# Optimization experiments

Measured on AMD Instinct MI355X. Metric: run time of the kernel, lower is better.

Reference implementation:

```python
import jax, jax.numpy as jnp
import numpy as np

CH = 512
HEADS = 4
GROUPS = 32  # _groups(512) -> 32
EPS = 1e-5


def setup_inputs() -> dict:
    key = jax.random.key(0)
    ks = jax.random.split(key, 7)
    b, c, h, w = 16, CH, 32, 32
    sd = 1.0 / np.sqrt(c)
    return {
        "x": jax.random.normal(ks[0], (b, c, h, w), dtype=jnp.float32),
        "gamma": jnp.ones((c,), jnp.float32),
        "beta": jnp.zeros((c,), jnp.float32),
        "w_qkv": jax.random.normal(ks[1], (3 * c, c), dtype=jnp.float32) * sd,
        "b_qkv": jax.random.normal(ks[2], (3 * c,), dtype=jnp.float32) * 0.01,
        "w_proj": jax.random.normal(ks[3], (c, c), dtype=jnp.float32) * sd,
        "b_proj": jax.random.normal(ks[4], (c,), dtype=jnp.float32) * 0.01,
    }


def _group_norm(x, gamma, beta):
    b, c, h, w = x.shape
    xg = x.reshape(b, GROUPS, -1)  # (b, G, c//G * h * w)
    mu = jnp.mean(xg, axis=-1, keepdims=True)
    var = jnp.var(xg, axis=-1, keepdims=True)
    xn = ((xg - mu) * jax.lax.rsqrt(var + EPS)).reshape(b, c, h, w)
    return xn * gamma[None, :, None, None] + beta[None, :, None, None]


def reference(x, gamma, beta, w_qkv, b_qkv, w_proj, b_proj):
    b, c, h, w = x.shape
    hd = c // HEADS
    xn = _group_norm(x, gamma, beta)
    # 1x1 conv == channel matmul
    qkv = jnp.einsum('oc,bchw->bohw', w_qkv, xn) + b_qkv[None, :, None, None]
    qkv = qkv.reshape(b, 3, HEADS, hd, h * w)
    q, k, v = qkv[:, 0], qkv[:, 1], qkv[:, 2]  # (b, H, hd, n)
    scale = hd ** -0.5
    attn = jax.nn.softmax(jnp.einsum('bhcn,bhcm->bhnm', q * scale, k), axis=-1)
    out = jnp.einsum('bhnm,bhcm->bhcn', attn, v).reshape(b, c, h, w)
    out = jnp.einsum('oc,bchw->bohw', w_proj, out) + b_proj[None, :, None, None]
    return x + out
```

## Files before the change

kernel.cpp:

```cpp
#include <hip/hip_runtime.h>

#define CH 512
#define HEADS 4
#define HD 128
#define NPIX 1024
#define BATCH 16
#define GROUPS 32
#define GSZ 16
#define EPS 1e-5f

typedef _Float16 f16;
typedef _Float16 f16x8 __attribute__((ext_vector_type(8)));
typedef _Float16 f16x4 __attribute__((ext_vector_type(4)));
typedef float f32x4 __attribute__((ext_vector_type(4)));

__device__ __forceinline__ void gld16(const f16* g, f16* l) {
    __builtin_amdgcn_global_load_lds((__attribute__((address_space(1))) const void*)g,
                                     (__attribute__((address_space(3))) void*)l, 16, 0, 0);
}

__global__ __launch_bounds__(256, 2) void k_pre(const float* __restrict__ x, const float* __restrict__ gamma,
                                                const float* __restrict__ beta, f16* __restrict__ xnT,
                                                const float* __restrict__ wq, const float* __restrict__ wp,
                                                f16* __restrict__ wqT, f16* __restrict__ wpT) {
    __shared__ float xs[GSZ * NPIX];
    __shared__ float red[8];
    __shared__ float stat2[2];
    int bidx = blockIdx.x;
    if (bidx >= 512) {
        int c = (bidx - 512) * 256 + threadIdx.x;
        {
            int ot = c >> 13, kbl = (c >> 7) & 63, ol = c & 127;
            const float* s = wq + ((size_t)(ot * 128 + ol)) * CH + kbl * 8;
            f32x4 a = *(const f32x4*)s, b2 = *(const f32x4*)(s + 4);
            f16x8 v;
            v[0] = (f16)a.x; v[1] = (f16)a.y; v[2] = (f16)a.z; v[3] = (f16)a.w;
            v[4] = (f16)b2.x; v[5] = (f16)b2.y; v[6] = (f16)b2.z; v[7] = (f16)b2.w;
            *(f16x8*)(wqT + (size_t)c * 8) = v;
        }
        if (c < 32768) {
            int ot = c >> 13, kbl = (c >> 7) & 63, ol = c & 127;
            const float* s = wp + ((size_t)(ot * 128 + ol)) * CH + kbl * 8;
            f32x4 a = *(const f32x4*)s, b2 = *(const f32x4*)(s + 4);
            f16x8 v;
            v[0] = (f16)a.x; v[1] = (f16)a.y; v[2] = (f16)a.z; v[3] = (f16)a.w;
            v[4] = (f16)b2.x; v[5] = (f16)b2.y; v[6] = (f16)b2.z; v[7] = (f16)b2.w;
            *(f16x8*)(wpT + (size_t)c * 8) = v;
        }
        return;
    }
    int g = bidx & 31, b = bidx >> 5;
    const f32x4* x4 = (const f32x4*)(x + ((size_t)(b * GROUPS + g)) * (GSZ * NPIX));
    float s = 0.f, ss = 0.f;
    for (int i = threadIdx.x; i < GSZ * NPIX / 4; i += 256) {
        f32x4 v = x4[i];
        *(f32x4*)&xs[i * 4] = v;
        s  += v.x + v.y + v.z + v.w;
        ss += v.x * v.x + v.y * v.y + v.z * v.z + v.w * v.w;
    }
    for (int off = 32; off; off >>= 1) { s += __shfl_down(s, off); ss += __shfl_down(ss, off); }
    int wv = threadIdx.x >> 6, ln = threadIdx.x & 63;
    if (ln == 0) { red[wv] = s; red[4 + wv] = ss; }
    __syncthreads();
    if (threadIdx.x == 0) {
        float S = red[0] + red[1] + red[2] + red[3];
        float SS = red[4] + red[5] + red[6] + red[7];
        float mu = S / (GSZ * NPIX);
        float var = SS / (GSZ * NPIX) - mu * mu;
        stat2[0] = mu; stat2[1] = rsqrtf(var + EPS);
    }
    __syncthreads();
    float mu = stat2[0], rstd = stat2[1];
    int ch = threadIdx.x >> 7;
    int n  = threadIdx.x & 127;
    float gl[8], bl[8];
#pragma unroll
    for (int i = 0; i < 8; i++) {
        float gv = gamma[g * 16 + ch * 8 + i] * rstd;
        gl[i] = gv;
        bl[i] = beta[g * 16 + ch * 8 + i] - mu * gv;
    }
    f16* tb0 = xnT + ((size_t)(b * 8)) * 65536 + (g * 2 + ch) * 1024 + n * 8;
#pragma unroll
    for (int nt = 0; nt < 8; nt++) {
        f16x8 o;
#pragma unroll
        for (int i = 0; i < 8; i++)
            o[i] = (f16)(xs[(ch * 8 + i) * 1024 + nt * 128 + n] * gl[i] + bl[i]);
        *(f16x8*)(tb0 + (size_t)nt * 65536) = o;
    }
}

__global__ __launch_bounds__(256, 3) void k_qkv(const f16* __restrict__ wT, const float* __restrict__ bias,
                                                const f16* __restrict__ xnT, f16* __restrict__ qF,
                                                f16* __restrict__ kTl, f16* __restrict__ vTl) {
    int nt = blockIdx.x, ot = blockIdx.y, b = blockIdx.z;
    int o0 = ot * 128;
    __shared__ union SM {
        struct { f16 As[8192]; f16 Bs[8192]; } s;
        f16 Cf[16384];
    } sm;
    __shared__ float biasS[128];
    if (threadIdx.x < 128) biasS[threadIdx.x] = bias[o0 + threadIdx.x];
    int tid = threadIdx.x, lane = tid & 63, wv = tid >> 6;
    int wr = wv >> 1, wc = wv & 1;
    int l15 = lane & 15, quad = lane >> 4;
    const f16* wA = wT + (size_t)ot * 65536;
    const f16* xB = xnT + ((size_t)(b * 8 + nt)) * 65536;
    f32x4 acc[4][4] = {};
    for (int kk = 0; kk < CH; kk += 64) {
        __syncthreads();
        const f16* sa = wA + (size_t)(kk >> 3) * 1024;
        const f16* sb = xB + (size_t)(kk >> 3) * 1024;
#pragma unroll
        for (int i = 0; i < 4; i++) {
            int s = wv * 4 + i;
            gld16(sa + (size_t)(s * 64 + lane) * 8, sm.s.As + s * 512);
            gld16(sb + (size_t)(s * 64 + lane) * 8, sm.s.Bs + s * 512);
        }
        __syncthreads();
#pragma unroll
        for (int dk = 0; dk < 2; dk++) {
            f16x8 af[4], bf[4];
#pragma unroll
            for (int t = 0; t < 4; t++) {
                af[t] = *(const f16x8*)(sm.s.As + (dk * 4 + quad) * 1024 + (wr * 64 + t * 16 + l15) * 8);
                bf[t] = *(const f16x8*)(sm.s.Bs + (dk * 4 + quad) * 1024 + (wc * 64 + t * 16 + l15) * 8);
            }
#pragma unroll
            for (int tm = 0; tm < 4; tm++)
#pragma unroll
                for (int tn = 0; tn < 4; tn++)
                    acc[tm][tn] = __builtin_amdgcn_mfma_f32_16x16x32_f16(af[tm], bf[tn], acc[tm][tn], 0, 0, 0);
        }
    }
    __syncthreads();
    int which = ot >> 2, h = ot & 3;
#pragma unroll
    for (int tm = 0; tm < 4; tm++)
#pragma unroll
        for (int tn = 0; tn < 4; tn++) {
            int ob = wr * 64 + tm * 16 + quad * 4;
            int n  = wc * 64 + tn * 16 + l15;
            f16x4 pv;
#pragma unroll
            for (int r = 0; r < 4; r++) pv[r] = (f16)(acc[tm][tn][r] + biasS[ob + r]);
            if (which == 0) {
                int addr = ((((n >> 5) * 2 + ((n >> 4) & 1)) * 4 + (ob >> 5)) * 512)
                         + ((ob >> 3) & 3) * 128 + (n & 15) * 8 + (quad & 1) * 4;
                *(f16x4*)&sm.Cf[addr] = pv;
            } else if (which == 1) {
                int addr = (ob >> 3) * 1024 + n * 8 + (quad & 1) * 4;
                *(f16x4*)&sm.Cf[addr] = pv;
            } else {
#pragma unroll
                for (int r = 0; r < 4; r++)
                    sm.Cf[(n >> 3) * 1024 + (ob + r) * 8 + (n & 7)] = pv[r];
            }
        }
    __syncthreads();
    f16* tb = (which == 0) ? (qF + ((size_t)((b * 4 + h) * 8 + nt)) * 16384)
            : (which == 1) ? (kTl + ((size_t)((b * 4 + h) * 8 + nt)) * 16384)
                           : (vTl + ((size_t)((b * 4 + h) * 8 + nt)) * 16384);
#pragma unroll
    for (int i = 0; i < 8; i++) {
        int cid = tid + i * 256;
        *(f16x8*)(tb + (size_t)cid * 8) = *(const f16x8*)(sm.Cf + cid * 8);
    }
}

__global__ __launch_bounds__(512, 1) void k_attn(const f16* __restrict__ qF, const f16* __restrict__ kTl,
                                                 const f16* __restrict__ vTl, f16* __restrict__ oT) {
    int bid = blockIdx.x;
    int ntp = bid >> 6, group = bid & 63;
    int b = group >> 2, h = group & 3;
    extern __shared__ f16 smem[];
    f16* Kl = smem;
    f16* Vl = smem + 16384;
    f16* PA = smem + 32768;
    f16* PB = smem + 49152;
    int tid = threadIdx.x, lane = tid & 63, wv = tid >> 6;
    int wq = wv & 3;
    int tile = wv >> 2;
    int nt = ntp * 2 + tile;
    int l15 = lane & 15, quad = lane >> 4;
    const f16* qb = qF + ((size_t)(group * 8 + nt)) * 16384;
    const f16* kb = kTl + (size_t)group * 8 * 16384;
    const f16* vb = vTl + (size_t)group * 8 * 16384;
    f16* Preg = tile ? PB : PA;

    f16x8 aq[2][4];
#pragma unroll
    for (int t = 0; t < 2; t++)
#pragma unroll
        for (int dk = 0; dk < 4; dk++) {
            int seg = (wq * 2 + t) * 4 + dk;
            f16x8 v = *(const f16x8*)(qb + seg * 512 + lane * 8);
            aq[t][dk] = v * (f16)0.08838834764831845f;
        }

    float m_i[2] = {-1e30f, -1e30f}, l_i[2] = {0.f, 0.f};
    f32x4 oaccT[2][8] = {};

    const f16* sbase = tile ? vb : kb;
    f16* dstL = tile ? Vl : Kl;
    f16x8 buf[8];
#pragma unroll
    for (int i = 0; i < 8; i++)
        buf[i] = *(const f16x8*)(sbase + (size_t)((wq * 8 + i) * 64 + lane) * 8);

    for (int mc = 0; mc < 8; mc++) {
        __syncthreads();
#pragma unroll
        for (int i = 0; i < 8; i++)
            *(f16x8*)&dstL[(wq * 8 + i) * 512 + lane * 8] = buf[i];
        __syncthreads();

        f32x4 st[2][8] = {};
#pragma unroll
        for (int dk = 0; dk < 4; dk++) {
            f16x8 kf[8];
#pragma unroll
            for (int t = 0; t < 8; t++)
                kf[t] = *(const f16x8*)&Kl[(dk * 4 + quad) * 1024 + (t * 16 + l15) * 8];
#pragma unroll
            for (int tr = 0; tr < 2; tr++)
#pragma unroll
                for (int tc = 0; tc < 8; tc++)
                    st[tr][tc] = __builtin_amdgcn_mfma_f32_16x16x32_f16(kf[tc], aq[tr][dk], st[tr][tc], 0, 0, 0);
        }

#pragma unroll
        for (int tr = 0; tr < 2; tr++) {
            float a[8];
#pragma unroll
            for (int tc = 0; tc < 8; tc++)
                a[tc] = fmaxf(fmaxf(st[tr][tc][0], st[tr][tc][1]), fmaxf(st[tr][tc][2], st[tr][tc][3]));
#pragma unroll
            for (int s = 4; s; s >>= 1)
#pragma unroll
                for (int k = 0; k < 4; k++) if (k < s) a[k] = fmaxf(a[k], a[k + s]);
            float mx = a[0];
            mx = fmaxf(mx, __shfl_xor(mx, 16));
            mx = fmaxf(mx, __shfl_xor(mx, 32));
            float mnew = fmaxf(m_i[tr], mx);
            float alpha = __expf(m_i[tr] - mnew);
            m_i[tr] = mnew;
            float r4[8];
#pragma unroll
            for (int tc = 0; tc < 8; tc++) {
                float p0 = __expf(st[tr][tc][0] - mnew);
                float p1 = __expf(st[tr][tc][1] - mnew);
                float p2 = __expf(st[tr][tc][2] - mnew);
                float p3 = __expf(st[tr][tc][3] - mnew);
                st[tr][tc][0] = p0; st[tr][tc][1] = p1;
                st[tr][tc][2] = p2; st[tr][tc][3] = p3;
                r4[tc] = (p0 + p1) + (p2 + p3);
            }
#pragma unroll
            for (int s = 4; s; s >>= 1)
#pragma unroll
                for (int k = 0; k < 4; k++) if (k < s) r4[k] += r4[k + s];
            float rs = r4[0];
            rs += __shfl_xor(rs, 16);
            rs += __shfl_xor(rs, 32);
            l_i[tr] = l_i[tr] * alpha + rs;
#pragma unroll
            for (int tc = 0; tc < 8; tc++) {
                oaccT[tr][tc].x *= alpha; oaccT[tr][tc].y *= alpha;
                oaccT[tr][tc].z *= alpha; oaccT[tr][tc].w *= alpha;
            }
        }

#pragma unroll
        for (int tr = 0; tr < 2; tr++) {
            int n = wq * 32 + tr * 16 + l15;
#pragma unroll
            for (int tc = 0; tc < 8; tc++) {
                int blk = tc * 2 + (quad >> 1);
                f16x4 pv;
#pragma unroll
                for (int r = 0; r < 4; r++) pv[r] = (f16)st[tr][tc][r];
                *(f16x4*)&Preg[n * 128 + ((blk ^ (n & 15)) << 3) + ((quad & 1) << 2)] = pv;
            }
        }

        if (mc < 7) {
            const f16* s = sbase + (size_t)(mc + 1) * 16384;
#pragma unroll
            for (int i = 0; i < 8; i++)
                buf[i] = *(const f16x8*)(s + (size_t)((wq * 8 + i) * 64 + lane) * 8);
        }

#pragma unroll
        for (int mk = 0; mk < 4; mk++) {
            f16x8 vf[8], pf[2];
#pragma unroll
            for (int t = 0; t < 8; t++)
                vf[t] = *(const f16x8*)&Vl[(mk * 4 + quad) * 1024 + (t * 16 + l15) * 8];
#pragma unroll
            for (int tr = 0; tr < 2; tr++) {
                int n = wq * 32 + tr * 16 + l15;
                int blk = mk * 4 + quad;
                pf[tr] = *(const f16x8*)&Preg[n * 128 + ((blk ^ (n & 15)) << 3)];
            }
#pragma unroll
            for (int tr = 0; tr < 2; tr++)
#pragma unroll
                for (int tc = 0; tc < 8; tc++)
                    oaccT[tr][tc] = __builtin_amdgcn_mfma_f32_16x16x32_f16(vf[tc], pf[tr], oaccT[tr][tc], 0, 0, 0);
        }
    }

#pragma unroll
    for (int tr = 0; tr < 2; tr++) {
        float inv = 1.f / l_i[tr];
        int n = wq * 32 + tr * 16 + l15;
#pragma unroll
        for (int tc = 0; tc < 8; tc++) {
            int blk = tc * 2 + (quad >> 1);
            f16x4 ov;
#pragma unroll
            for (int r = 0; r < 4; r++) ov[r] = (f16)(oaccT[tr][tc][r] * inv);
            *(f16x4*)&Preg[n * 128 + ((blk ^ (n & 15)) << 3) + ((quad & 1) << 2)] = ov;
        }
    }
    __syncthreads();
    f16* ob = oT + ((size_t)(b * 8 + nt)) * 65536;
    int t256 = tid & 255;
#pragma unroll
    for (int i = 0; i < 8; i++) {
        int cid = t256 + i * 256;
        int cbl = cid >> 7, n = cid & 127;
        f16x8 v = *(const f16x8*)&Preg[n * 128 + ((cbl ^ (n & 15)) << 3)];
        *(f16x8*)(ob + (size_t)(h * 16 + cbl) * 1024 + n * 8) = v;
    }
}

__global__ __launch_bounds__(256, 3) void k_proj(const f16* __restrict__ wT, const float* __restrict__ bias,
                                                 const f16* __restrict__ oT, const float* __restrict__ x,
                                                 float* __restrict__ out) {
    int nt = blockIdx.x, ot = blockIdx.y, b = blockIdx.z;
    int n0 = nt * 128, o0 = ot * 128;
    __shared__ union SM {
        struct { f16 As[8192]; f16 Bs[8192]; } s;
        f16 Cs[128][136];
    } sm;
    __shared__ float biasS[128];
    if (threadIdx.x < 128) biasS[threadIdx.x] = bias[o0 + threadIdx.x];
    int tid = threadIdx.x, lane = tid & 63, wv = tid >> 6;
    int wr = wv >> 1, wc = wv & 1;
    int l15 = lane & 15, quad = lane >> 4;
    const f16* wA = wT + (size_t)ot * 65536;
    const f16* xB = oT + ((size_t)(b * 8 + nt)) * 65536;
    f32x4 acc[4][4] = {};
    for (int kk = 0; kk < CH; kk += 64) {
        __syncthreads();
        const f16* sa = wA + (size_t)(kk >> 3) * 1024;
        const f16* sb = xB + (size_t)(kk >> 3) * 1024;
#pragma unroll
        for (int i = 0; i < 4; i++) {
            int s = wv * 4 + i;
            gld16(sa + (size_t)(s * 64 + lane) * 8, sm.s.As + s * 512);
            gld16(sb + (size_t)(s * 64 + lane) * 8, sm.s.Bs + s * 512);
        }
        __syncthreads();
#pragma unroll
        for (int dk = 0; dk < 2; dk++) {
            f16x8 af[4], bf[4];
#pragma unroll
            for (int t = 0; t < 4; t++) {
                af[t] = *(const f16x8*)(sm.s.As + (dk * 4 + quad) * 1024 + (wr * 64 + t * 16 + l15) * 8);
                bf[t] = *(const f16x8*)(sm.s.Bs + (dk * 4 + quad) * 1024 + (wc * 64 + t * 16 + l15) * 8);
            }
#pragma unroll
            for (int tm = 0; tm < 4; tm++)
#pragma unroll
                for (int tn = 0; tn < 4; tn++)
                    acc[tm][tn] = __builtin_amdgcn_mfma_f32_16x16x32_f16(af[tm], bf[tn], acc[tm][tn], 0, 0, 0);
        }
    }
    __syncthreads();
#pragma unroll
    for (int tm = 0; tm < 4; tm++)
#pragma unroll
        for (int tn = 0; tn < 4; tn++)
#pragma unroll
            for (int r = 0; r < 4; r++) {
                int o = wr * 64 + tm * 16 + quad * 4 + r;
                int n = wc * 64 + tn * 16 + l15;
                sm.Cs[o][n] = (f16)(acc[tm][tn][r] + biasS[o]);
            }
    __syncthreads();
#pragma unroll
    for (int i = 0; i < 8; i++) {
        int cid = tid + i * 256;
        int row = cid >> 4, off = (cid & 15) * 8;
        f16x8 v = *(const f16x8*)&sm.Cs[row][off];
        size_t gofs = ((size_t)(b * CH) + o0 + row) * NPIX + n0 + off;
        const float* xp = x + gofs;
        float* op = out + gofs;
        f32x4 o0v, o1v;
        o0v.x = xp[0] + (float)v[0]; o0v.y = xp[1] + (float)v[1];
        o0v.z = xp[2] + (float)v[2]; o0v.w = xp[3] + (float)v[3];
        o1v.x = xp[4] + (float)v[4]; o1v.y = xp[5] + (float)v[5];
        o1v.z = xp[6] + (float)v[6]; o1v.w = xp[7] + (float)v[7];
        *(f32x4*)op = o0v; *(f32x4*)(op + 4) = o1v;
    }
}

extern "C" void kernel_launch(void* const* d_in, const int* in_sizes, int n_in,
                              void* d_out, int out_size, void* d_ws, size_t ws_size,
                              hipStream_t stream) {
    const float* x     = (const float*)d_in[0];
    const float* gamma = (const float*)d_in[1];
    const float* beta  = (const float*)d_in[2];
    const float* wqkv  = (const float*)d_in[3];
    const float* bqkv  = (const float*)d_in[4];
    const float* wproj = (const float*)d_in[5];
    const float* bproj = (const float*)d_in[6];
    float* out = (float*)d_out;

    char* p = (char*)d_ws;
    f16* wqT = (f16*)p;           p += (size_t)3 * CH * CH * 2;
    f16* wpT = (f16*)p;           p += (size_t)CH * CH * 2;
    f16* xnT = (f16*)p;           p += (size_t)BATCH * NPIX * CH * 2;
    f16* qF  = (f16*)p;           p += (size_t)BATCH * HEADS * NPIX * HD * 2;
    f16* kTl = (f16*)p;           p += (size_t)BATCH * HEADS * NPIX * HD * 2;
    f16* vTl = (f16*)p;           p += (size_t)BATCH * HEADS * NPIX * HD * 2;
    f16* oT  = (f16*)p;           p += (size_t)BATCH * NPIX * CH * 2;

    k_pre<<<dim3(896), 256, 0, stream>>>(x, gamma, beta, xnT, wqkv, wproj, wqT, wpT);
    k_qkv<<<dim3(8, 12, BATCH), 256, 0, stream>>>(wqT, bqkv, xnT, qF, kTl, vTl);

    hipFuncSetAttribute((const void*)k_attn, hipFuncAttributeMaxDynamicSharedMemorySize, 131072);
    k_attn<<<dim3(256), 512, 131072, stream>>>(qF, kTl, vTl, oT);

    k_proj<<<dim3(8, 4, BATCH), 256, 0, stream>>>(wpT, bproj, oT, x, out);
}
```

Baseline: 208.4 us.

## Shrink attention blocks to one query tile with half-size KV chunks for higher occupancy

The attention kernel now gives each 512-thread block a single 128-query tile, with each wave owning 16 query rows instead of 32. Keys and values stream in 64-key chunks over 16 iterations rather than 128-key chunks over 8. Static shared memory drops to 48KB and launch bounds allow 4 blocks per CU, doubling the grid to 512 blocks. The aim is more resident waves and less register and LDS pressure to hide latency, at the cost of more barriers per query tile and K/V being re-read from global memory by twice as many blocks.

```diff
diff --git a/kernel.cpp b/kernel.cpp
--- a/kernel.cpp
+++ b/kernel.cpp
@@ -169,170 +169,152 @@
     }
 }
 
-__global__ __launch_bounds__(512, 1) void k_attn(const f16* __restrict__ qF, const f16* __restrict__ kTl,
+__global__ __launch_bounds__(512, 4) void k_attn(const f16* __restrict__ qF, const f16* __restrict__ kTl,
                                                  const f16* __restrict__ vTl, f16* __restrict__ oT) {
+    __shared__ f16 smem[24576];
+    f16* Kl = smem;
+    f16* Vl = smem + 8192;
     int bid = blockIdx.x;
-    int ntp = bid >> 6, group = bid & 63;
+    int nt = bid >> 6, group = bid & 63;
     int b = group >> 2, h = group & 3;
-    extern __shared__ f16 smem[];
-    f16* Kl = smem;
-    f16* Vl = smem + 16384;
-    f16* PA = smem + 32768;
-    f16* PB = smem + 49152;
     int tid = threadIdx.x, lane = tid & 63, wv = tid >> 6;
-    int wq = wv & 3;
-    int tile = wv >> 2;
-    int nt = ntp * 2 + tile;
+    int wq = wv & 3, role = wv >> 2;
     int l15 = lane & 15, quad = lane >> 4;
     const f16* qb = qF + ((size_t)(group * 8 + nt)) * 16384;
     const f16* kb = kTl + (size_t)group * 8 * 16384;
     const f16* vb = vTl + (size_t)group * 8 * 16384;
-    f16* Preg = tile ? PB : PA;
-
-    f16x8 aq[2][4];
-#pragma unroll
-    for (int t = 0; t < 2; t++)
+    f16* Preg = smem + 16384 + wv * 1024;
+    f16* dstL = role ? Vl : Kl;
+
+    f16x8 aq[4];
+#pragma unroll
+    for (int dk = 0; dk < 4; dk++) {
+        f16x8 v = *(const f16x8*)(qb + (wv * 4 + dk) * 512 + lane * 8);
+        aq[dk] = v * (f16)0.08838834764831845f;
+    }
+
+    float m_i = -1e30f, l_i = 0.f;
+    f32x4 oaccT[8] = {};
+
+    f16x8 buf[4];
+    if (role == 0) {
+#pragma unroll
+        for (int i = 0; i < 4; i++)
+            buf[i] = *(const f16x8*)(kb + (size_t)(wq * 4 + i) * 1024 + lane * 8);
+    } else {
+#pragma unroll
+        for (int i = 0; i < 4; i++)
+            buf[i] = *(const f16x8*)(vb + (size_t)(wq * 4 + i) * 512 + lane * 8);
+    }
+
+    for (int mc = 0; mc < 16; mc++) {
+        __syncthreads();
+#pragma unroll
+        for (int i = 0; i < 4; i++)
+            *(f16x8*)&dstL[(wq * 4 + i) * 512 + lane * 8] = buf[i];
+        __syncthreads();
+
+        f32x4 st[4] = {};
 #pragma unroll
         for (int dk = 0; dk < 4; dk++) {
-            int seg = (wq * 2 + t) * 4 + dk;
-            f16x8 v = *(const f16x8*)(qb + seg * 512 + lane * 8);
-            aq[t][dk] = v * (f16)0.08838834764831845f;
-        }
-
-    float m_i[2] = {-1e30f, -1e30f}, l_i[2] = {0.f, 0.f};
-    f32x4 oaccT[2][8] = {};
-
-    const f16* sbase = tile ? vb : kb;
-    f16* dstL = tile ? Vl : Kl;
-    f16x8 buf[8];
-#pragma unroll
-    for (int i = 0; i < 8; i++)
-        buf[i] = *(const f16x8*)(sbase + (size_t)((wq * 8 + i) * 64 + lane) * 8);
-
-    for (int mc = 0; mc < 8; mc++) {
-        __syncthreads();
-#pragma unroll
-        for (int i = 0; i < 8; i++)
-            *(f16x8*)&dstL[(wq * 8 + i) * 512 + lane * 8] = buf[i];
-        __syncthreads();
-
-        f32x4 st[2][8] = {};
-#pragma unroll
-        for (int dk = 0; dk < 4; dk++) {
-            f16x8 kf[8];
-#pragma unroll
-            for (int t = 0; t < 8; t++)
-                kf[t] = *(const f16x8*)&Kl[(dk * 4 + quad) * 1024 + (t * 16 + l15) * 8];
-#pragma unroll
-            for (int tr = 0; tr < 2; tr++)
-#pragma unroll
-                for (int tc = 0; tc < 8; tc++)
-                    st[tr][tc] = __builtin_amdgcn_mfma_f32_16x16x32_f16(kf[tc], aq[tr][dk], st[tr][tc], 0, 0, 0);
-        }
-
-#pragma unroll
-        for (int tr = 0; tr < 2; tr++) {
-            float a[8];
-#pragma unroll
-            for (int tc = 0; tc < 8; tc++)
-                a[tc] = fmaxf(fmaxf(st[tr][tc][0], st[tr][tc][1]), fmaxf(st[tr][tc][2], st[tr][tc][3]));
-#pragma unroll
-            for (int s = 4; s; s >>= 1)
-#pragma unroll
-                for (int k = 0; k < 4; k++) if (k < s) a[k] = fmaxf(a[k], a[k + s]);
-            float mx = a[0];
-            mx = fmaxf(mx, __shfl_xor(mx, 16));
-            mx = fmaxf(mx, __shfl_xor(mx, 32));
-            float mnew = fmaxf(m_i[tr], mx);
-            float alpha = __expf(m_i[tr] - mnew);
-            m_i[tr] = mnew;
-            float r4[8];
-#pragma unroll
-            for (int tc = 0; tc < 8; tc++) {
-                float p0 = __expf(st[tr][tc][0] - mnew);
-                float p1 = __expf(st[tr][tc][1] - mnew);
-                float p2 = __expf(st[tr][tc][2] - mnew);
-                float p3 = __expf(st[tr][tc][3] - mnew);
-                st[tr][tc][0] = p0; st[tr][tc][1] = p1;
-                st[tr][tc][2] = p2; st[tr][tc][3] = p3;
-                r4[tc] = (p0 + p1) + (p2 + p3);
+            f16x8 kf[4];
+#pragma unroll
+            for (int t = 0; t < 4; t++)
+                kf[t] = *(const f16x8*)&Kl[(dk * 4 + quad) * 512 + (t * 16 + l15) * 8];
+#pragma unroll
+            for (int tc = 0; tc < 4; tc++)
+                st[tc] = __builtin_amdgcn_mfma_f32_16x16x32_f16(kf[tc], aq[dk], st[tc], 0, 0, 0);
+        }
+
+        float a[4];
+#pragma unroll
+        for (int tc = 0; tc < 4; tc++)
+            a[tc] = fmaxf(fmaxf(st[tc][0], st[tc][1]), fmaxf(st[tc][2], st[tc][3]));
+        a[0] = fmaxf(a[0], a[2]); a[1] = fmaxf(a[1], a[3]);
+        float mx = fmaxf(a[0], a[1]);
+        mx = fmaxf(mx, __shfl_xor(mx, 16));
+        mx = fmaxf(mx, __shfl_xor(mx, 32));
+        float mnew = fmaxf(m_i, mx);
+        float alpha = __expf(m_i - mnew);
+        m_i = mnew;
+        float r4[4];
+#pragma unroll
+        for (int tc = 0; tc < 4; tc++) {
+            float p0 = __expf(st[tc][0] - mnew);
+            float p1 = __expf(st[tc][1] - mnew);
+            float p2 = __expf(st[tc][2] - mnew);
+            float p3 = __expf(st[tc][3] - mnew);
+            st[tc][0] = p0; st[tc][1] = p1;
+            st[tc][2] = p2; st[tc][3] = p3;
+            r4[tc] = (p0 + p1) + (p2 + p3);
+        }
+        float rs = (r4[0] + r4[1]) + (r4[2] + r4[3]);
+        rs += __shfl_xor(rs, 16);
+        rs += __shfl_xor(rs, 32);
+        l_i = l_i * alpha + rs;
+#pragma unroll
+        for (int tc = 0; tc < 8; tc++) {
+            oaccT[tc].x *= alpha; oaccT[tc].y *= alpha;
+            oaccT[tc].z *= alpha; oaccT[tc].w *= alpha;
+        }
+
+#pragma unroll
+        for (int tc = 0; tc < 4; tc++) {
+            int blk = tc * 2 + (quad >> 1);
+            f16x4 pv;
+#pragma unroll
+            for (int r = 0; r < 4; r++) pv[r] = (f16)st[tc][r];
+            *(f16x4*)&Preg[l15 * 64 + ((blk ^ (l15 & 7)) << 3) + ((quad & 1) << 2)] = pv;
+        }
+
+        if (mc < 15) {
+            if (role == 0) {
+                const f16* s = kb + (size_t)((mc + 1) >> 1) * 16384 + (size_t)((mc + 1) & 1) * 512;
+#pragma unroll
+                for (int i = 0; i < 4; i++)
+                    buf[i] = *(const f16x8*)(s + (size_t)(wq * 4 + i) * 1024 + lane * 8);
+            } else {
+                const f16* s = vb + (size_t)(mc + 1) * 8192;
+#pragma unroll
+                for (int i = 0; i < 4; i++)
+                    buf[i] = *(const f16x8*)(s + (size_t)(wq * 4 + i) * 512 + lane * 8);
             }
-#pragma unroll
-            for (int s = 4; s; s >>= 1)
-#pragma unroll
-                for (int k = 0; k < 4; k++) if (k < s) r4[k] += r4[k + s];
-            float rs = r4[0];
-            rs += __shfl_xor(rs, 16);
-            rs += __shfl_xor(rs, 32);
-            l_i[tr] = l_i[tr] * alpha + rs;
-#pragma unroll
-            for (int tc = 0; tc < 8; tc++) {
-                oaccT[tr][tc].x *= alpha; oaccT[tr][tc].y *= alpha;
-                oaccT[tr][tc].z *= alpha; oaccT[tr][tc].w *= alpha;
-            }
-        }
-
-#pragma unroll
-        for (int tr = 0; tr < 2; tr++) {
-            int n = wq * 32 + tr * 16 + l15;
-#pragma unroll
-            for (int tc = 0; tc < 8; tc++) {
-                int blk = tc * 2 + (quad >> 1);
-                f16x4 pv;
-#pragma unroll
-                for (int r = 0; r < 4; r++) pv[r] = (f16)st[tr][tc][r];
-                *(f16x4*)&Preg[n * 128 + ((blk ^ (n & 15)) << 3) + ((quad & 1) << 2)] = pv;
-            }
-        }
-
-        if (mc < 7) {
-            const f16* s = sbase + (size_t)(mc + 1) * 16384;
-#pragma unroll
-            for (int i = 0; i < 8; i++)
-                buf[i] = *(const f16x8*)(s + (size_t)((wq * 8 + i) * 64 + lane) * 8);
-        }
-
-#pragma unroll
-        for (int mk = 0; mk < 4; mk++) {
-            f16x8 vf[8], pf[2];
+        }
+
+#pragma unroll
+        for (int mk = 0; mk < 2; mk++) {
+            f16x8 vf[8];
 #pragma unroll
             for (int t = 0; t < 8; t++)
                 vf[t] = *(const f16x8*)&Vl[(mk * 4 + quad) * 1024 + (t * 16 + l15) * 8];
-#pragma unroll
-            for (int tr = 0; tr < 2; tr++) {
-                int n = wq * 32 + tr * 16 + l15;
-                int blk = mk * 4 + quad;
-                pf[tr] = *(const f16x8*)&Preg[n * 128 + ((blk ^ (n & 15)) << 3)];
-            }
-#pragma unroll
-            for (int tr = 0; tr < 2; tr++)
-#pragma unroll
-                for (int tc = 0; tc < 8; tc++)
-                    oaccT[tr][tc] = __builtin_amdgcn_mfma_f32_16x16x32_f16(vf[tc], pf[tr], oaccT[tr][tc], 0, 0, 0);
-        }
-    }
-
-#pragma unroll
-    for (int tr = 0; tr < 2; tr++) {
-        float inv = 1.f / l_i[tr];
-        int n = wq * 32 + tr * 16 + l15;
+            int blk = mk * 4 + quad;
+            f16x8 pf = *(const f16x8*)&Preg[l15 * 64 + ((blk ^ (l15 & 7)) << 3)];
+#pragma unroll
+            for (int tc = 0; tc < 8; tc++)
+                oaccT[tc] = __builtin_amdgcn_mfma_f32_16x16x32_f16(vf[tc], pf, oaccT[tc], 0, 0, 0);
+        }
+    }
+
+    __syncthreads();
+    {
+        float inv = 1.f / l_i;
+        int n = wv * 16 + l15;
 #pragma unroll
         for (int tc = 0; tc < 8; tc++) {
             int blk = tc * 2 + (quad >> 1);
             f16x4 ov;
 #pragma unroll
-            for (int r = 0; r < 4; r++) ov[r] = (f16)(oaccT[tr][tc][r] * inv);
-            *(f16x4*)&Preg[n * 128 + ((blk ^ (n & 15)) << 3) + ((quad & 1) << 2)] = ov;
+            for (int r = 0; r < 4; r++) ov[r] = (f16)(oaccT[tc][r] * inv);
+            *(f16x4*)&smem[n * 128 + ((blk ^ (n & 15)) << 3) + ((quad & 1) << 2)] = ov;
         }
     }
     __syncthreads();
     f16* ob = oT + ((size_t)(b * 8 + nt)) * 65536;
-    int t256 = tid & 255;
-#pragma unroll
-    for (int i = 0; i < 8; i++) {
-        int cid = t256 + i * 256;
+#pragma unroll
+    for (int i = 0; i < 4; i++) {
+        int cid = tid + i * 512;
         int cbl = cid >> 7, n = cid & 127;
-        f16x8 v = *(const f16x8*)&Preg[n * 128 + ((cbl ^ (n & 15)) << 3)];
+        f16x8 v = *(const f16x8*)&smem[n * 128 + ((cbl ^ (n & 15)) << 3)];
         *(f16x8*)(ob + (size_t)(h * 16 + cbl) * 1024 + n * 8) = v;
     }
 }
@@ -432,9 +414,6 @@
 
     k_pre<<<dim3(896), 256, 0, stream>>>(x, gamma, beta, xnT, wqkv, wproj, wqT, wpT);
     k_qkv<<<dim3(8, 12, BATCH), 256, 0, stream>>>(wqT, bqkv, xnT, qF, kTl, vTl);
-
-    hipFuncSetAttribute((const void*)k_attn, hipFuncAttributeMaxDynamicSharedMemorySize, 131072);
-    k_attn<<<dim3(256), 512, 131072, stream>>>(qF, kTl, vTl, oT);
-
+    k_attn<<<dim3(512), 512, 0, stream>>>(qF, kTl, vTl, oT);
     k_proj<<<dim3(8, 4, BATCH), 256, 0, stream>>>(wpT, bproj, oT, x, out);
 }
```

Result: faster. 196.1 us (-5.9%).
